# Performance work log

Hardware: AMD Instinct MI355X
Metric: run time of the kernel (lower is better)

The kernel has to match this reference:

```python
import jax, jax.numpy as jnp
import numpy as np

N = 50000        # nodes
E_RAND = 800000  # random edges (self-loops appended -> E = 850000)
H = 8            # num_heads
D = 32           # h_feat_dim
IN = 128         # in_feat_dim
SM = 256         # sm_dim
SP = 128         # sp_dim
NEG_SLOPE = 0.2  # DGL GATv2Conv default


def setup_inputs() -> dict:
    key = jax.random.key(0)
    ks = jax.random.split(key, 16)
    s = 0.05
    self_loops = jnp.arange(N, dtype=jnp.int32)
    return {
        "sm_feats": jax.random.normal(ks[0], (N, SM), jnp.float32),
        "sp_feats": jax.random.normal(ks[1], (N, SP), jnp.float32),
        "src": jnp.concatenate([jax.random.randint(ks[2], (E_RAND,), 0, N, jnp.int32), self_loops]),
        "dst": jnp.concatenate([jax.random.randint(ks[3], (E_RAND,), 0, N, jnp.int32), self_loops]),
        # T1 / T2 linears
        "T1_w": jax.random.normal(ks[4], (SM, IN), jnp.float32) * s,
        "T1_b": jnp.zeros((IN,), jnp.float32),
        "T2_w": jax.random.normal(ks[5], (SP, IN), jnp.float32) * s,
        "T2_b": jnp.zeros((IN,), jnp.float32),
        # GATv2 layer 1: in = 2*IN
        "g1_src_w": jax.random.normal(ks[6], (2 * IN, H * D), jnp.float32) * s,
        "g1_dst_w": jax.random.normal(ks[7], (2 * IN, H * D), jnp.float32) * s,
        "g1_attn": jax.random.normal(ks[8], (H, D), jnp.float32) * s,
        "g1_bias": jnp.zeros((H * D,), jnp.float32),
        # GATv2 layer 2: in = D (after head-mean)
        "g2_src_w": jax.random.normal(ks[9], (D, H * D), jnp.float32) * s,
        "g2_dst_w": jax.random.normal(ks[10], (D, H * D), jnp.float32) * s,
        "g2_attn": jax.random.normal(ks[11], (H, D), jnp.float32) * s,
        "g2_bias": jnp.zeros((H * D,), jnp.float32),
    }


def gatv2_conv(x, src, dst, w_src, w_dst, attn, bias):
    # DGL GATv2Conv (share_weights=False, bias=True, no residual/activation)
    feat_src = (x @ w_src).reshape(-1, H, D)   # [N,H,D]
    feat_dst = (x @ w_dst).reshape(-1, H, D)   # [N,H,D]
    e = jax.nn.leaky_relu(feat_src[src] + feat_dst[dst], NEG_SLOPE)  # [E,H,D]
    score = jnp.einsum('ehd,hd->eh', e, attn)  # [E,H]
    # edge softmax over incoming edges per destination (self-loops ensure non-empty)
    smax = jax.ops.segment_max(score, dst, num_segments=N)           # [N,H]
    ex = jnp.exp(score - smax[dst])
    denom = jax.ops.segment_sum(ex, dst, num_segments=N)             # [N,H]
    alpha = ex / denom[dst]                                          # [E,H]
    out = jax.ops.segment_sum(alpha[:, :, None] * feat_src[src], dst, num_segments=N)  # [N,H,D]
    return out + bias.reshape(1, H, D)


def reference(sm_feats, sp_feats, src, dst,
              T1_w, T1_b, T2_w, T2_b,
              g1_src_w, g1_dst_w, g1_attn, g1_bias,
              g2_src_w, g2_dst_w, g2_attn, g2_bias):
    in_feat = jnp.concatenate([sm_feats @ T1_w + T1_b,
                               sp_feats @ T2_w + T2_b], axis=1)      # [N, 2*IN]
    h = gatv2_conv(in_feat, src, dst, g1_src_w, g1_dst_w, g1_attn, g1_bias)
    h = jax.nn.elu(h).mean(axis=1)                                   # [N, D]
    h = gatv2_conv(h, src, dst, g2_src_w, g2_dst_w, g2_attn, g2_bias)
    return h.mean(axis=1)                                            # [N, D]
```

## Files before the change

### kernel.cpp

```cpp
#include <hip/hip_runtime.h>
#include <hip/hip_fp16.h>


typedef unsigned int uint32;
typedef unsigned short u16;
typedef float f32x4 __attribute__((ext_vector_type(4)));
typedef _Float16 f16x2 __attribute__((ext_vector_type(2)));
typedef _Float16 f16x8 __attribute__((ext_vector_type(8)));

union H2 { f16x2 v; uint32 u; };

__device__ __forceinline__ int wave_incl_scan(int x) {
  int lane = threadIdx.x & 63;
#pragma unroll
  for (int off = 1; off < 64; off <<= 1) {
    int t = __shfl_up(x, off, 64);
    if (lane >= off) x += t;
  }
  return x;
}

__global__ __launch_bounds__(256) void k_deg(const int* __restrict__ dst, int* __restrict__ deg, int E) {
  int e = blockIdx.x * 256 + threadIdx.x;
  if (e < E) atomicAdd(&deg[dst[e]], 1);
}

__global__ __launch_bounds__(1024) void k_scan1(const int* __restrict__ deg, int* __restrict__ rp,
                                                int n, int Etot) {
  __shared__ int wpart[16];
  __shared__ int sbase;
  int tid = threadIdx.x, lane = tid & 63, wid = tid >> 6;
  if (tid == 0) sbase = 0;
  __syncthreads();
  for (int c0 = 0; c0 < n; c0 += 4096) {
    int i0 = c0 + tid * 4;
    int v0 = 0, v1 = 0, v2 = 0, v3 = 0;
    if (i0 + 3 < n) {
      int4 t = *(const int4*)(deg + i0);
      v0 = t.x; v1 = t.y; v2 = t.z; v3 = t.w;
    } else {
      if (i0 < n) v0 = deg[i0];
      if (i0 + 1 < n) v1 = deg[i0 + 1];
      if (i0 + 2 < n) v2 = deg[i0 + 2];
      if (i0 + 3 < n) v3 = deg[i0 + 3];
    }
    int ts = v0 + v1 + v2 + v3;
    int incl = wave_incl_scan(ts);
    if (lane == 63) wpart[wid] = incl;
    __syncthreads();
    if (wid == 0 && lane < 16) {
      int xv = wpart[lane];
#pragma unroll
      for (int off = 1; off < 16; off <<= 1) {
        int t = __shfl_up(xv, off, 64);
        if (lane >= off) xv += t;
      }
      wpart[lane] = xv;
    }
    __syncthreads();
    int tot = wpart[15];
    int base = sbase + (wid ? wpart[wid - 1] : 0);
    int excl = base + incl - ts;
    if (i0 + 3 < n) {
      int4 o; o.x = excl; o.y = excl + v0; o.z = excl + v0 + v1; o.w = excl + v0 + v1 + v2;
      *(int4*)(rp + i0) = o;
    } else {
      if (i0 < n) rp[i0] = excl;
      if (i0 + 1 < n) rp[i0 + 1] = excl + v0;
      if (i0 + 2 < n) rp[i0 + 2] = excl + v0 + v1;
      if (i0 + 3 < n) rp[i0 + 3] = excl + v0 + v1 + v2;
    }
    __syncthreads();
    if (tid == 0) sbase += tot;
  }
  if (tid == 0) rp[n] = Etot;
}

__global__ __launch_bounds__(256) void k_fill(const int* __restrict__ src, const int* __restrict__ dst,
                                              const int* __restrict__ rp, int* __restrict__ cnt,
                                              int* __restrict__ csr_src, int E) {
  int e = blockIdx.x * 256 + threadIdx.x;
  if (e < E) {
    int d = dst[e];
    int p = rp[d] + atomicAdd(&cnt[d], 1);
    csr_src[p] = src[e];
  }
}

__global__ __launch_bounds__(256) void k_precomb(const float* __restrict__ T1w, const float* __restrict__ T1b,
                                                 const float* __restrict__ T2w, const float* __restrict__ T2b,
                                                 const float* __restrict__ G1, const float* __restrict__ G2,
                                                 __half* __restrict__ Bf, float* __restrict__ cvec) {
  int bb = blockIdx.x;
  const float* G = (bb < 385) ? G1 : G2;
  int off = (bb < 385) ? 0 : 256;
  int r = (bb < 385) ? bb : bb - 385;
  int j = threadIdx.x;
  float acc = 0.f;
  if (r < 256) {
    for (int m = 0; m < 128; m++) acc += T1w[r * 128 + m] * G[m * 256 + j];
  } else if (r < 384) {
    int rr = r - 256;
    for (int m = 0; m < 128; m++) acc += T2w[rr * 128 + m] * G[(128 + m) * 256 + j];
  } else {
    for (int m = 0; m < 128; m++) acc += T1b[m] * G[m * 256 + j] + T2b[m] * G[(128 + m) * 256 + j];
    cvec[off + j] = acc;
    return;
  }
  int k = r, colabs = off + j;
  int kt = k >> 5, lq = (k >> 3) & 3, j8 = k & 7;
  int cb = colabs >> 7, colr = colabs & 127, ni = colr >> 4, lr = colr & 15;
  size_t idx = ((size_t)(((cb * 12 + kt) * 8 + ni) * 4 + lq) * 16 + lr) * 8 + j8;
  Bf[idx] = __float2half(acc);
}

__global__ __launch_bounds__(256, 4) void k_gemm(const float* __restrict__ sm, const float* __restrict__ sp,
                                                 const u16* __restrict__ Bf, const float* __restrict__ cvec,
                                                 __half* __restrict__ fs, __half* __restrict__ fd, int N) {
  int tid = threadIdx.x, w = tid >> 6, l = tid & 63;
  int lr = l & 15, lq = l >> 4;
  int L = blockIdx.x;
  int x = L & 7, m = L >> 3;
  int cb = m & 3;
  int rb = x + 8 * (m >> 2);
  int col0 = cb * 128, row0 = rb * 128;
  if (row0 >= N) return;
  int r0 = row0 + w * 32 + lr;
  int r1 = r0 + 16;
  int c0 = r0 < N ? r0 : N - 1;
  int c1 = r1 < N ? r1 : N - 1;
  const float* psm0 = sm + (size_t)c0 * 256 + lq * 8;
  const float* psm1 = sm + (size_t)c1 * 256 + lq * 8;
  const float* psp0 = sp + (size_t)c0 * 128 + lq * 8;
  const float* psp1 = sp + (size_t)c1 * 128 + lq * 8;
  const u16* bp = Bf + (size_t)cb * 49152 + (size_t)l * 8;

  f32x4 acc[2][8];
#pragma unroll
  for (int mt = 0; mt < 2; mt++)
#pragma unroll
    for (int ni = 0; ni < 8; ni++) acc[mt][ni] = (f32x4){0.f, 0.f, 0.f, 0.f};

#define LOADA(P, D)                                                     \
  {                                                                     \
    const float* _g0 = ((P) < 8) ? (psm0 + (P)*32) : (psp0 + ((P)-8) * 32); \
    const float* _g1 = ((P) < 8) ? (psm1 + (P)*32) : (psp1 + ((P)-8) * 32); \
    D[0] = *(const float4*)_g0;                                         \
    D[1] = *(const float4*)(_g0 + 4);                                   \
    D[2] = *(const float4*)_g1;                                         \
    D[3] = *(const float4*)(_g1 + 4);                                   \
  }

  float4 Aa[4], Ab[4];
  LOADA(0, Aa);

#pragma unroll
  for (int st = 0; st < 12; st++) {
    const float4* Dc = (st & 1) ? Ab : Aa;
    float4* Dn = (st & 1) ? Aa : Ab;
    if (st < 11) LOADA(st + 1, Dn);
    f16x8 a0, a1;
    a0[0] = (_Float16)Dc[0].x; a0[1] = (_Float16)Dc[0].y;
    a0[2] = (_Float16)Dc[0].z; a0[3] = (_Float16)Dc[0].w;
    a0[4] = (_Float16)Dc[1].x; a0[5] = (_Float16)Dc[1].y;
    a0[6] = (_Float16)Dc[1].z; a0[7] = (_Float16)Dc[1].w;
    a1[0] = (_Float16)Dc[2].x; a1[1] = (_Float16)Dc[2].y;
    a1[2] = (_Float16)Dc[2].z; a1[3] = (_Float16)Dc[2].w;
    a1[4] = (_Float16)Dc[3].x; a1[5] = (_Float16)Dc[3].y;
    a1[6] = (_Float16)Dc[3].z; a1[7] = (_Float16)Dc[3].w;
#pragma unroll
    for (int ni = 0; ni < 8; ni++) {
      f16x8 bf = *(const f16x8*)(bp + st * 4096 + ni * 512);
      acc[0][ni] = __builtin_amdgcn_mfma_f32_16x16x32_f16(a0, bf, acc[0][ni], 0, 0, 0);
      acc[1][ni] = __builtin_amdgcn_mfma_f32_16x16x32_f16(a1, bf, acc[1][ni], 0, 0, 0);
    }
  }

#pragma unroll
  for (int mt = 0; mt < 2; mt++) {
    int rbr = row0 + w * 32 + mt * 16 + lq * 4;
#pragma unroll
    for (int ni = 0; ni < 8; ni++) {
      int c = col0 + ni * 16 + lr;
      float cv = cvec[c];
      __half* op = fs; int cc = c;
      if (c >= 256) { op = fd; cc = c - 256; }
#pragma unroll
      for (int r = 0; r < 4; r++) {
        int rr = rbr + r;
        if (rr < N) op[(size_t)rr * 256 + cc] = __float2half(acc[mt][ni][r] + cv);
      }
    }
  }
#undef LOADA
}

__global__ __launch_bounds__(256) void k_feat2(const float* __restrict__ h, const float* __restrict__ Ws,
                                               const float* __restrict__ Wd, __half* __restrict__ fs,
                                               __half* __restrict__ fd, int N) {
  int j = threadIdx.x;
  int n0 = blockIdx.x * 32;
  float ws[32], wd[32];
#pragma unroll
  for (int k = 0; k < 32; k++) {
    ws[k] = Ws[k * 256 + j];
    wd[k] = Wd[k * 256 + j];
  }
  int nend = n0 + 32; if (nend > N) nend = N;
#pragma unroll 2
  for (int n = n0; n < nend; n++) {
    const float* hr = h + (size_t)n * 32;
    float as = 0.f, ad = 0.f;
#pragma unroll
    for (int k = 0; k < 32; k++) {
      float hv = hr[k];
      as += hv * ws[k];
      ad += hv * wd[k];
    }
    fs[(size_t)n * 256 + j] = __float2half(as);
    fd[(size_t)n * 256 + j] = __float2half(ad);
  }
}

template <int FINAL>
__global__ __launch_bounds__(256) void k_edge(const uint4* __restrict__ fs4, const uint4* __restrict__ fd4,
                                              const int* __restrict__ csr_src, const int* __restrict__ rp,
                                              const float* __restrict__ attn, const float* __restrict__ bias,
                                              float* __restrict__ out, int N) {
  int n = blockIdx.x * 4 + (threadIdx.x >> 6);
  if (n >= N) return;
  int lane = threadIdx.x & 63;
  int lh = lane & 31;
  float4 a0 = ((const float4*)attn)[lh * 2];
  float4 a1 = ((const float4*)attn)[lh * 2 + 1];
  H2 AV01, AV23, AV45, AV67;
  AV01.v = (f16x2){(_Float16)a0.x, (_Float16)a0.y};
  AV23.v = (f16x2){(_Float16)a0.z, (_Float16)a0.w};
  AV45.v = (f16x2){(_Float16)a1.x, (_Float16)a1.y};
  AV67.v = (f16x2){(_Float16)a1.z, (_Float16)a1.w};
  const f16x2 c02 = {(_Float16)0.2f, (_Float16)0.2f};
  uint4 yu = fd4[(size_t)n * 32 + lh];
  H2 Y01, Y23, Y45, Y67;
  Y01.u = yu.x; Y23.u = yu.y; Y45.u = yu.z; Y67.u = yu.w;
  int beg = rp[n], end = rp[n + 1];
  float den = 0.f;
  float acc[8] = {0.f, 0.f, 0.f, 0.f, 0.f, 0.f, 0.f, 0.f};

  auto pair1 = [&](uint4 xu, bool tail) {
    H2 Xa, Xb, Xc, Xd;
    Xa.u = xu.x; Xb.u = xu.y; Xc.u = xu.z; Xd.u = xu.w;
    f16x2 e0 = Xa.v + Y01.v, e1 = Xb.v + Y23.v, e2 = Xc.v + Y45.v, e3 = Xd.v + Y67.v;
    f16x2 t0 = __builtin_elementwise_max(e0, e0 * c02);
    f16x2 t1 = __builtin_elementwise_max(e1, e1 * c02);
    f16x2 t2 = __builtin_elementwise_max(e2, e2 * c02);
    f16x2 t3 = __builtin_elementwise_max(e3, e3 * c02);
    float p = __builtin_amdgcn_fdot2(t0, AV01.v, 0.f, false);
    p = __builtin_amdgcn_fdot2(t1, AV23.v, p, false);
    p = __builtin_amdgcn_fdot2(t2, AV45.v, p, false);
    p = __builtin_amdgcn_fdot2(t3, AV67.v, p, false);
    p += __shfl_xor(p, 1, 64);
    p += __shfl_xor(p, 2, 64);
    float wgt = __expf(p);
    if (tail && lane >= 32) wgt = 0.f;
    den += wgt;
    acc[0] += wgt * (float)Xa.v.x; acc[1] += wgt * (float)Xa.v.y;
    acc[2] += wgt * (float)Xb.v.x; acc[3] += wgt * (float)Xb.v.y;
    acc[4] += wgt * (float)Xc.v.x; acc[5] += wgt * (float)Xc.v.y;
    acc[6] += wgt * (float)Xd.v.x; acc[7] += wgt * (float)Xd.v.y;
  };

  int e = beg;
  int np = (end - beg) >> 1;
  if (np > 0) {
    int sA = csr_src[e], sB = csr_src[e + 1];
    int s = (lane < 32) ? sA : sB;
    uint4 xcur = fs4[(size_t)s * 32 + lh];
    for (int q = 1; q < np; q++) {
      int eb = e + 2 * q;
      int tA = csr_src[eb], tB = csr_src[eb + 1];
      int t = (lane < 32) ? tA : tB;
      uint4 xnext = fs4[(size_t)t * 32 + lh];
      pair1(xcur, false);
      xcur = xnext;
    }
    pair1(xcur, false);
    e += 2 * np;
  }
  if (e < end) {
    int sA = csr_src[e];
    uint4 xu = fs4[(size_t)sA * 32 + lh];
    pair1(xu, true);
  }

  den += __shfl_xor(den, 32, 64);
#pragma unroll
  for (int j = 0; j < 8; j++) acc[j] += __shfl_xor(acc[j], 32, 64);
  float invd = 1.f / den;
  float4 b0 = ((const float4*)bias)[lh * 2];
  float4 b1 = ((const float4*)bias)[lh * 2 + 1];
  float bj[8] = {b0.x, b0.y, b0.z, b0.w, b1.x, b1.y, b1.z, b1.w};
#pragma unroll
  for (int j = 0; j < 8; j++) {
    float v = acc[j] * invd + bj[j];
    if (!FINAL) v = v > 0.f ? v : expm1f(v);
    acc[j] = v;
  }
#pragma unroll
  for (int mask = 4; mask <= 16; mask <<= 1)
#pragma unroll
    for (int j = 0; j < 8; j++) acc[j] += __shfl_xor(acc[j], mask, 64);
  if (lane < 4) {
    float4 o0 = {acc[0] * 0.125f, acc[1] * 0.125f, acc[2] * 0.125f, acc[3] * 0.125f};
    float4 o1 = {acc[4] * 0.125f, acc[5] * 0.125f, acc[6] * 0.125f, acc[7] * 0.125f};
    ((float4*)out)[(size_t)n * 8 + lane * 2] = o0;
    ((float4*)out)[(size_t)n * 8 + lane * 2 + 1] = o1;
  }
}

extern "C" void kernel_launch(void* const* d_in, const int* in_sizes, int n_in,
                              void* d_out, int out_size, void* d_ws, size_t ws_size,
                              hipStream_t stream) {
  const float* sm  = (const float*)d_in[0];
  const float* sp  = (const float*)d_in[1];
  const int*   src = (const int*)d_in[2];
  const int*   dst = (const int*)d_in[3];
  const float* T1w = (const float*)d_in[4];
  const float* T1b = (const float*)d_in[5];
  const float* T2w = (const float*)d_in[6];
  const float* T2b = (const float*)d_in[7];
  const float* g1sw = (const float*)d_in[8];
  const float* g1dw = (const float*)d_in[9];
  const float* g1a  = (const float*)d_in[10];
  const float* g1b  = (const float*)d_in[11];
  const float* g2sw = (const float*)d_in[12];
  const float* g2dw = (const float*)d_in[13];
  const float* g2a  = (const float*)d_in[14];
  const float* g2b  = (const float*)d_in[15];
  const int N = in_sizes[1] / 128;
  const int E = in_sizes[2];
  float* out = (float*)d_out;

  size_t off = 0;
  char* wsb = (char*)d_ws;
  auto alloc = [&](size_t bytes) -> void* {
    void* p = wsb + off;
    off += (bytes + 255) & ~(size_t)255;
    return p;
  };
  __half* Bf  = (__half*)alloc((size_t)512 * 384 * 2);
  float* cvec  = (float*)alloc(512 * 4);
  int* deg     = (int*)alloc((size_t)N * 4);
  int* cnt     = (int*)alloc((size_t)N * 4);
  int* row_ptr = (int*)alloc((size_t)(N + 1) * 4);
  int* csr_src = (int*)alloc((size_t)E * 4);
  __half* fs   = (__half*)alloc((size_t)N * 256 * 2);
  __half* fd   = (__half*)alloc((size_t)N * 256 * 2);
  float* hmid  = (float*)alloc((size_t)N * 32 * 4);
  (void)ws_size; (void)n_in; (void)out_size;

  (void)hipMemsetAsync(deg, 0, (size_t)N * 4, stream);
  (void)hipMemsetAsync(cnt, 0, (size_t)N * 4, stream);

  k_deg<<<(E + 255) / 256, 256, 0, stream>>>(dst, deg, E);
  k_scan1<<<1, 1024, 0, stream>>>(deg, row_ptr, N, E);
  k_fill<<<(E + 255) / 256, 256, 0, stream>>>(src, dst, row_ptr, cnt, csr_src, E);

  k_precomb<<<770, 256, 0, stream>>>(T1w, T1b, T2w, T2b, g1sw, g1dw, Bf, cvec);

  int rbs = (N + 127) / 128;
  int rbp = (rbs + 7) & ~7;
  k_gemm<<<dim3(rbp * 4), 256, 0, stream>>>(sm, sp, (const u16*)Bf, cvec, fs, fd, N);
  k_edge<0><<<(N + 3) / 4, 256, 0, stream>>>((const uint4*)fs, (const uint4*)fd, csr_src, row_ptr, g1a, g1b, hmid, N);

  k_feat2<<<(N + 31) / 32, 256, 0, stream>>>(hmid, g2sw, g2dw, fs, fd, N);
  k_edge<1><<<(N + 3) / 4, 256, 0, stream>>>((const uint4*)fs, (const uint4*)fd, csr_src, row_ptr, g2a, g2b, out, N);
}
```

Before: 481.8 us.

## Stage GEMM A and B tiles through LDS with async global-to-LDS loads

Rewrites the fused T1/T2 + GAT projection GEMM so that B fragments are staged into a triple-buffered LDS ring using global_load_lds. A tiles are loaded cooperatively with coalesced float4 reads, converted to fp16 and written into a swizzled double-buffered LDS tile. Previously each wave read B straight from global memory and loaded A with strided per-lane reads. The change is meant to cut redundant global traffic across the four waves and improve coalescing, at the cost of per-stage barriers, hand-placed waitcnts and more LDS use, which may reduce occupancy.

```diff
diff --git a/kernel.cpp b/kernel.cpp
--- a/kernel.cpp
+++ b/kernel.cpp
@@ -6,6 +6,7 @@
 typedef unsigned short u16;
 typedef float f32x4 __attribute__((ext_vector_type(4)));
 typedef _Float16 f16x2 __attribute__((ext_vector_type(2)));
+typedef _Float16 f16x4 __attribute__((ext_vector_type(4)));
 typedef _Float16 f16x8 __attribute__((ext_vector_type(8)));
 
 union H2 { f16x2 v; uint32 u; };
@@ -114,9 +115,16 @@
   Bf[idx] = __float2half(acc);
 }
 
+#define GLL(GP, LP)                                                     \
+  __builtin_amdgcn_global_load_lds(                                     \
+      (const __attribute__((address_space(1))) void*)(GP),              \
+      (__attribute__((address_space(3))) void*)(LP), 16, 0, 0)
+
 __global__ __launch_bounds__(256, 4) void k_gemm(const float* __restrict__ sm, const float* __restrict__ sp,
                                                  const u16* __restrict__ Bf, const float* __restrict__ cvec,
                                                  __half* __restrict__ fs, __half* __restrict__ fd, int N) {
+  __shared__ u16 BFl[3 * 4096];
+  __shared__ u16 AFl[2 * 4096];
   int tid = threadIdx.x, w = tid >> 6, l = tid & 63;
   int lr = l & 15, lq = l >> 4;
   int L = blockIdx.x;
@@ -125,15 +133,20 @@
   int rb = x + 8 * (m >> 2);
   int col0 = cb * 128, row0 = rb * 128;
   if (row0 >= N) return;
-  int r0 = row0 + w * 32 + lr;
-  int r1 = r0 + 16;
-  int c0 = r0 < N ? r0 : N - 1;
-  int c1 = r1 < N ? r1 : N - 1;
-  const float* psm0 = sm + (size_t)c0 * 256 + lq * 8;
-  const float* psm1 = sm + (size_t)c1 * 256 + lq * 8;
-  const float* psp0 = sp + (size_t)c0 * 128 + lq * 8;
-  const float* psp1 = sp + (size_t)c1 * 128 + lq * 8;
-  const u16* bp = Bf + (size_t)cb * 49152 + (size_t)l * 8;
+
+  int o_sm[4], o_sp[4], woff[4];
+#pragma unroll
+  for (int i = 0; i < 4; i++) {
+    int idx = i * 256 + tid;
+    int r = idx >> 3, c8 = idx & 7;
+    int rg = row0 + r; if (rg >= N) rg = N - 1;
+    o_sm[i] = rg * 256 + c8 * 4;
+    o_sp[i] = rg * 128 + c8 * 4;
+    woff[i] = r * 32 + ((c8 * 4) ^ ((r & 6) << 2));
+  }
+  int r0l = w * 32 + lr, r1l = r0l + 16;
+  int ra0 = r0l * 32 + ((lq * 8) ^ ((r0l & 6) << 2));
+  int ra1 = r1l * 32 + ((lq * 8) ^ ((r1l & 6) << 2));
 
   f32x4 acc[2][8];
 #pragma unroll
@@ -141,38 +154,68 @@
 #pragma unroll
     for (int ni = 0; ni < 8; ni++) acc[mt][ni] = (f32x4){0.f, 0.f, 0.f, 0.f};
 
-#define LOADA(P, D)                                                     \
+#define STAGE_B(S, BUF)                                                 \
   {                                                                     \
-    const float* _g0 = ((P) < 8) ? (psm0 + (P)*32) : (psp0 + ((P)-8) * 32); \
-    const float* _g1 = ((P) < 8) ? (psm1 + (P)*32) : (psp1 + ((P)-8) * 32); \
-    D[0] = *(const float4*)_g0;                                         \
-    D[1] = *(const float4*)(_g0 + 4);                                   \
-    D[2] = *(const float4*)_g1;                                         \
-    D[3] = *(const float4*)(_g1 + 4);                                   \
-  }
-
-  float4 Aa[4], Ab[4];
-  LOADA(0, Aa);
+    size_t g0 = (size_t)(cb * 12 + (S)) * 4096;                         \
+    _Pragma("unroll") for (int i = 0; i < 2; i++) {                     \
+      int c = i * 256 + tid;                                            \
+      int lb = (BUF)*4096 + (i * 4 + w) * 512;                          \
+      GLL(Bf + g0 + (size_t)c * 8, &BFl[lb]);                           \
+    }                                                                   \
+  }
+
+#define ALOAD(S)                                                        \
+  {                                                                     \
+    _Pragma("unroll") for (int i = 0; i < 4; i++) {                     \
+      const float* g = ((S) < 8) ? (sm + o_sm[i] + (S)*32) : (sp + o_sp[i] + ((S)-8) * 32); \
+      D[i] = *(const float4*)g;                                         \
+    }                                                                   \
+  }
+
+#define AWRITE(SLOT)                                                    \
+  {                                                                     \
+    _Pragma("unroll") for (int i = 0; i < 4; i++) {                     \
+      f16x4 h;                                                          \
+      h[0] = (_Float16)D[i].x; h[1] = (_Float16)D[i].y;                 \
+      h[2] = (_Float16)D[i].z; h[3] = (_Float16)D[i].w;                 \
+      *(f16x4*)&AFl[(SLOT)*4096 + woff[i]] = h;                         \
+    }                                                                   \
+  }
+
+  float4 D[4];
+  ALOAD(0);
+  STAGE_B(0, 0);
+  STAGE_B(1, 1);
+  asm volatile("s_waitcnt vmcnt(4)" ::: "memory");
+  AWRITE(0);
+  asm volatile("s_waitcnt vmcnt(2)" ::: "memory");
+  asm volatile("s_waitcnt lgkmcnt(0)" ::: "memory");
+  __builtin_amdgcn_sched_barrier(0);
+  __builtin_amdgcn_s_barrier();
 
 #pragma unroll
   for (int st = 0; st < 12; st++) {
-    const float4* Dc = (st & 1) ? Ab : Aa;
-    float4* Dn = (st & 1) ? Aa : Ab;
-    if (st < 11) LOADA(st + 1, Dn);
-    f16x8 a0, a1;
-    a0[0] = (_Float16)Dc[0].x; a0[1] = (_Float16)Dc[0].y;
-    a0[2] = (_Float16)Dc[0].z; a0[3] = (_Float16)Dc[0].w;
-    a0[4] = (_Float16)Dc[1].x; a0[5] = (_Float16)Dc[1].y;
-    a0[6] = (_Float16)Dc[1].z; a0[7] = (_Float16)Dc[1].w;
-    a1[0] = (_Float16)Dc[2].x; a1[1] = (_Float16)Dc[2].y;
-    a1[2] = (_Float16)Dc[2].z; a1[3] = (_Float16)Dc[2].w;
-    a1[4] = (_Float16)Dc[3].x; a1[5] = (_Float16)Dc[3].y;
-    a1[6] = (_Float16)Dc[3].z; a1[7] = (_Float16)Dc[3].w;
+    const int cu = st & 1, nx = cu ^ 1, bs = st % 3;
+    if (st < 11) ALOAD(st + 1);
+    if (st < 10) STAGE_B(st + 2, (st + 2) % 3);
+    f16x8 a0 = *(const f16x8*)&AFl[cu * 4096 + ra0];
+    f16x8 a1 = *(const f16x8*)&AFl[cu * 4096 + ra1];
 #pragma unroll
     for (int ni = 0; ni < 8; ni++) {
-      f16x8 bf = *(const f16x8*)(bp + st * 4096 + ni * 512);
+      f16x8 bf = *(const f16x8*)&BFl[bs * 4096 + (ni * 64 + l) * 8];
       acc[0][ni] = __builtin_amdgcn_mfma_f32_16x16x32_f16(a0, bf, acc[0][ni], 0, 0, 0);
       acc[1][ni] = __builtin_amdgcn_mfma_f32_16x16x32_f16(a1, bf, acc[1][ni], 0, 0, 0);
+    }
+    if (st < 10) {
+      asm volatile("s_waitcnt vmcnt(2)" ::: "memory");
+    } else if (st == 10) {
+      asm volatile("s_waitcnt vmcnt(0)" ::: "memory");
+    }
+    if (st < 11) {
+      AWRITE(nx);
+      asm volatile("s_waitcnt lgkmcnt(0)" ::: "memory");
+      __builtin_amdgcn_sched_barrier(0);
+      __builtin_amdgcn_s_barrier();
     }
   }
 
@@ -192,7 +235,9 @@
       }
     }
   }
-#undef LOADA
+#undef STAGE_B
+#undef ALOAD
+#undef AWRITE
 }
 
 __global__ __launch_bounds__(256) void k_feat2(const float* __restrict__ h, const float* __restrict__ Ws,
```

Result: faster. 460.9 us (-4.4%).
